# Kernel optimization log

Measured on AMD Instinct MI355X. Metric: run time of the kernel, lower is better.

The kernel has to match this reference:

```python
import jax, jax.numpy as jnp
import numpy as np

TEMPERATURE = 0.5
EPS = 1e-8  # matches torch cosine_similarity eps guard semantics (norm clamp)


def setup_inputs() -> dict:
    key = jax.random.key(0)
    k1, k2 = jax.random.split(key)
    B, D = 4096, 256
    z_i = jax.random.normal(k1, (B, D), dtype=jnp.float32)
    z_j = jax.random.normal(k2, (B, D), dtype=jnp.float32)
    return {"z_i": z_i, "z_j": z_j}


def reference(z_i, z_j):
    B = z_i.shape[0]
    z = jnp.concatenate([z_i, z_j], axis=0)            # [2B, D]
    # cosine similarity: normalize once, then GEMM
    norm = jnp.maximum(jnp.linalg.norm(z, axis=1, keepdims=True), EPS)
    zn = z / norm                                       # [2B, D]
    sim = zn @ zn.T                                     # [2B, 2B]
    # positives: diag(sim, +B) and diag(sim, -B)
    idx = jnp.arange(B)
    sim_ij = sim[idx, idx + B]
    sim_ji = sim[idx + B, idx]
    positives = jnp.concatenate([sim_ij, sim_ji])       # [2B]
    # masked denominator: exclude self-similarity
    mask = 1.0 - jnp.eye(2 * B, dtype=sim.dtype)
    denom = jnp.sum(mask * jnp.exp(sim / TEMPERATURE), axis=1)  # [2B]
    all_losses = -jnp.log(jnp.exp(positives / TEMPERATURE) / denom)
    return jnp.sum(all_losses) / (2 * B)
```

## Files before the change

### kernel.cpp

```cpp
#include <hip/hip_runtime.h>
#include <hip/hip_bf16.h>
#include <cstdint>
#include <cstddef>
#include <math.h>

#define D 256
#define TEMP_INV 2.0f
#define EPS_NORM 1e-8f
#define NTILES 2080

typedef __attribute__((ext_vector_type(8))) short bf16x8;
typedef __attribute__((ext_vector_type(4))) float f32x4;

__global__ void __launch_bounds__(256) normalize_rows(
    const float* __restrict__ zi, const float* __restrict__ zj,
    __hip_bfloat16* __restrict__ zn, float* __restrict__ out, int B) {
  const int wid = threadIdx.x >> 6;
  const int lane = threadIdx.x & 63;
  if (blockIdx.x == 0 && threadIdx.x == 0) out[0] = 0.0f;
#pragma unroll
  for (int it = 0; it < 4; ++it) {
    int row = it * 2048 + blockIdx.x * 4 + wid;
    const float* src = (row < B) ? (zi + (size_t)row * D)
                                 : (zj + (size_t)(row - B) * D);
    float4 v = ((const float4*)src)[lane];
    float ss = v.x * v.x + v.y * v.y + v.z * v.z + v.w * v.w;
    for (int off = 32; off; off >>= 1) ss += __shfl_xor(ss, off);
    float rn = 1.0f / fmaxf(sqrtf(ss), EPS_NORM);
    union { ushort4 u; __hip_bfloat16 h[4]; } o;
    o.h[0] = __float2bfloat16(v.x * rn);
    o.h[1] = __float2bfloat16(v.y * rn);
    o.h[2] = __float2bfloat16(v.z * rn);
    o.h[3] = __float2bfloat16(v.w * rn);
    ((ushort4*)zn)[(size_t)row * (D / 4) + lane] = o.u;
  }
}

__device__ __forceinline__ void decode_tile(int t, int Nb, int& by, int& bx) {
  float fb = (2.0f * Nb + 1.0f -
              sqrtf((float)((2 * Nb + 1) * (2 * Nb + 1) - 8 * t))) * 0.5f;
  int y = (int)fb;
  while ((y + 1) * Nb - ((y + 1) * y) / 2 <= t) ++y;
  while (y * Nb - (y * (y - 1)) / 2 > t) --y;
  by = y;
  bx = y + (t - (y * Nb - (y * (y - 1)) / 2));
}

__global__ void __launch_bounds__(256, 4) ntxent_gemm(
    const __hip_bfloat16* __restrict__ zn,
    float* __restrict__ part, float* __restrict__ pos, int B) {
  __shared__ __align__(16) __hip_bfloat16 Bsh[128 * 64];

  const int N = 2 * B;
  const int Nb = N / 128;
  int by, bx;
  decode_tile(blockIdx.x, Nb, by, bx);
  const int bm = by * 128;
  const int bn = bx * 128;
  const bool isDiag = (by == bx);
  const bool isPos = (bx == by + B / 128);

  const int tid = threadIdx.x;
  const int wid = tid >> 6;
  const int lane = tid & 63;
  const int wy = wid >> 1, wx = wid & 1;
  const int wrow0 = wid * 32;

  const int lr = lane >> 3;
  const int c8 = lane & 7;

  const int frow = lane & 15;
  const int quad = lane >> 4;
  const int f7 = frow & 7;

  f32x4 acc[4][4] = {};

  const __hip_bfloat16* gB = zn + (size_t)(bn + wrow0 + lr) * D + c8 * 8;
  const int ldsoff = (wrow0 + lr) * 64 + (c8 ^ lr) * 8;

  const __hip_bfloat16* gA = zn + (size_t)(bm + wy * 64 + frow) * D + quad * 8;

  float4 vb0 = *(const float4*)(gB + 0 * 8 * D);
  float4 vb1 = *(const float4*)(gB + 1 * 8 * D);
  float4 vb2 = *(const float4*)(gB + 2 * 8 * D);
  float4 vb3 = *(const float4*)(gB + 3 * 8 * D);

#pragma unroll
  for (int k0i = 0; k0i < 4; ++k0i) {
    __syncthreads();
    *(float4*)&Bsh[ldsoff + 0 * 8 * 64] = vb0;
    *(float4*)&Bsh[ldsoff + 1 * 8 * 64] = vb1;
    *(float4*)&Bsh[ldsoff + 2 * 8 * 64] = vb2;
    *(float4*)&Bsh[ldsoff + 3 * 8 * 64] = vb3;
    __syncthreads();
    if (k0i < 3) {
      const int k0 = (k0i + 1) * 64;
      vb0 = *(const float4*)(gB + 0 * 8 * D + k0);
      vb1 = *(const float4*)(gB + 1 * 8 * D + k0);
      vb2 = *(const float4*)(gB + 2 * 8 * D + k0);
      vb3 = *(const float4*)(gB + 3 * 8 * D + k0);
    }
#pragma unroll
    for (int kk = 0; kk < 2; ++kk) {
      const int kcol = k0i * 64 + kk * 32;
      bf16x8 a[4], b[4];
#pragma unroll
      for (int i = 0; i < 4; ++i)
        a[i] = *(const bf16x8*)(gA + (size_t)(i * 16) * D + kcol);
#pragma unroll
      for (int j = 0; j < 4; ++j)
        b[j] = *(const bf16x8*)
            &Bsh[(wx * 64 + j * 16 + frow) * 64 + ((kk * 4 + quad) ^ f7) * 8];
#pragma unroll
      for (int i = 0; i < 4; ++i)
#pragma unroll
        for (int j = 0; j < 4; ++j)
          acc[i][j] =
              __builtin_amdgcn_mfma_f32_16x16x32_bf16(a[i], b[j], acc[i][j], 0, 0, 0);
    }
  }

  __syncthreads();
  float* red = (float*)&Bsh[0];

  const int colq = lane & 15;
  float cs[4] = {0.0f, 0.0f, 0.0f, 0.0f};
#pragma unroll
  for (int i = 0; i < 4; ++i) {
#pragma unroll
    for (int r = 0; r < 4; ++r) {
      int rowloc = wy * 64 + i * 16 + quad * 4 + r;
      int row = bm + rowloc;
      float rs = 0.0f;
#pragma unroll
      for (int j = 0; j < 4; ++j) {
        int col = bn + wx * 64 + j * 16 + colq;
        float v = acc[i][j][r];
        float e = __expf(v * TEMP_INV);
        e = (isDiag && col == row) ? 0.0f : e;
        rs += e;
        cs[j] += e;
        if (isPos && col == row + B) { pos[row] = v; pos[col] = v; }
      }
      rs += __shfl_xor(rs, 1);
      rs += __shfl_xor(rs, 2);
      rs += __shfl_xor(rs, 4);
      rs += __shfl_xor(rs, 8);
      if (colq == 0) red[rowloc * 2 + wx] = rs;
    }
  }
#pragma unroll
  for (int j = 0; j < 4; ++j) {
    float c = cs[j];
    c += __shfl_xor(c, 16);
    c += __shfl_xor(c, 32);
    if (quad == 0) red[256 + (wx * 64 + j * 16 + colq) * 2 + wy] = c;
  }
  __syncthreads();
  if (tid < 128) {
    part[(size_t)bx * N + bm + tid] = red[tid * 2] + red[tid * 2 + 1];
  } else if (!isDiag) {
    int tt = tid - 128;
    part[(size_t)by * N + bn + tt] = red[256 + tt * 2] + red[256 + tt * 2 + 1];
  }
}

__global__ void __launch_bounds__(256) finalize(
    const float* __restrict__ part, const float* __restrict__ pos,
    float* __restrict__ out, int N) {
  const int idx = blockIdx.x * 256 + threadIdx.x;
  const int NS = N / 128;
  float s = 0.0f;
#pragma unroll 8
  for (int k = 0; k < NS; ++k) s += part[(size_t)k * N + idx];
  float loss = __logf(s) - pos[idx] * TEMP_INV;
  for (int off = 32; off; off >>= 1) loss += __shfl_xor(loss, off);
  __shared__ float redsh[4];
  if ((threadIdx.x & 63) == 0) redsh[threadIdx.x >> 6] = loss;
  __syncthreads();
  if (threadIdx.x == 0) {
    float tt = redsh[0] + redsh[1] + redsh[2] + redsh[3];
    atomicAdd(out, tt / (float)N);
  }
}

extern "C" void kernel_launch(void* const* d_in, const int* in_sizes, int n_in,
                              void* d_out, int out_size, void* d_ws, size_t ws_size,
                              hipStream_t stream) {
  const float* zi = (const float*)d_in[0];
  const float* zj = (const float*)d_in[1];
  const int B = in_sizes[0] / D;
  const int N = 2 * B;

  __hip_bfloat16* zn = (__hip_bfloat16*)d_ws;
  float* pos = (float*)((char*)d_ws + (size_t)N * D * sizeof(__hip_bfloat16));
  float* part = pos + N;

  normalize_rows<<<512, 256, 0, stream>>>(zi, zj, zn, (float*)d_out, B);
  ntxent_gemm<<<NTILES, 256, 0, stream>>>(zn, part, pos, B);
  finalize<<<N / 256, 256, 0, stream>>>(part, pos, (float*)d_out, N);
}
```

Baseline: 122.0 us.

## Drop LDS staging and write per-warp partial sums straight to global

The GEMM kernel stops staging the B tile through shared memory. Each warp now loads its B fragments directly from global memory, relying on the cache, and all __syncthreads barriers are gone. The row and column exp-sum reductions no longer pass through LDS. Each warp writes its partials to a partial-sum buffer twice as tall, and finalize sums N/64 slices instead of N/128. This removes barriers and LDS traffic, at the cost of redundant global/L2 reads of B across warps and twice the partial-sum writes and finalize reads, plus a larger workspace.

```diff
diff --git a/kernel.cpp b/kernel.cpp
--- a/kernel.cpp
+++ b/kernel.cpp
@@ -49,119 +49,83 @@
 __global__ void __launch_bounds__(256, 4) ntxent_gemm(
     const __hip_bfloat16* __restrict__ zn,
     float* __restrict__ part, float* __restrict__ pos, int B) {
-  __shared__ __align__(16) __hip_bfloat16 Bsh[128 * 64];
-
   const int N = 2 * B;
   const int Nb = N / 128;
   int by, bx;
   decode_tile(blockIdx.x, Nb, by, bx);
   const int bm = by * 128;
   const int bn = bx * 128;
-  const bool isDiag = (by == bx);
-  const bool isPos = (bx == by + B / 128);
 
   const int tid = threadIdx.x;
   const int wid = tid >> 6;
   const int lane = tid & 63;
   const int wy = wid >> 1, wx = wid & 1;
-  const int wrow0 = wid * 32;
-
-  const int lr = lane >> 3;
-  const int c8 = lane & 7;
 
   const int frow = lane & 15;
   const int quad = lane >> 4;
-  const int f7 = frow & 7;
+
+  const bool diagQ = (by == bx) && (wy == wx);
+  const bool posQ = (bx == by + B / 128) && (wy == wx);
+  const bool isDiag = (by == bx);
+
+  const __hip_bfloat16* gA = zn + (size_t)(bm + wy * 64 + frow) * D + quad * 8;
+  const __hip_bfloat16* gB = zn + (size_t)(bn + wx * 64 + frow) * D + quad * 8;
 
   f32x4 acc[4][4] = {};
 
-  const __hip_bfloat16* gB = zn + (size_t)(bn + wrow0 + lr) * D + c8 * 8;
-  const int ldsoff = (wrow0 + lr) * 64 + (c8 ^ lr) * 8;
-
-  const __hip_bfloat16* gA = zn + (size_t)(bm + wy * 64 + frow) * D + quad * 8;
-
-  float4 vb0 = *(const float4*)(gB + 0 * 8 * D);
-  float4 vb1 = *(const float4*)(gB + 1 * 8 * D);
-  float4 vb2 = *(const float4*)(gB + 2 * 8 * D);
-  float4 vb3 = *(const float4*)(gB + 3 * 8 * D);
-
 #pragma unroll
-  for (int k0i = 0; k0i < 4; ++k0i) {
-    __syncthreads();
-    *(float4*)&Bsh[ldsoff + 0 * 8 * 64] = vb0;
-    *(float4*)&Bsh[ldsoff + 1 * 8 * 64] = vb1;
-    *(float4*)&Bsh[ldsoff + 2 * 8 * 64] = vb2;
-    *(float4*)&Bsh[ldsoff + 3 * 8 * 64] = vb3;
-    __syncthreads();
-    if (k0i < 3) {
-      const int k0 = (k0i + 1) * 64;
-      vb0 = *(const float4*)(gB + 0 * 8 * D + k0);
-      vb1 = *(const float4*)(gB + 1 * 8 * D + k0);
-      vb2 = *(const float4*)(gB + 2 * 8 * D + k0);
-      vb3 = *(const float4*)(gB + 3 * 8 * D + k0);
-    }
+  for (int kc = 0; kc < 8; ++kc) {
+    const int kcol = kc * 32;
+    bf16x8 a[4], b[4];
 #pragma unroll
-    for (int kk = 0; kk < 2; ++kk) {
-      const int kcol = k0i * 64 + kk * 32;
-      bf16x8 a[4], b[4];
+    for (int i = 0; i < 4; ++i)
+      a[i] = *(const bf16x8*)(gA + (size_t)(i * 16) * D + kcol);
 #pragma unroll
-      for (int i = 0; i < 4; ++i)
-        a[i] = *(const bf16x8*)(gA + (size_t)(i * 16) * D + kcol);
+    for (int j = 0; j < 4; ++j)
+      b[j] = *(const bf16x8*)(gB + (size_t)(j * 16) * D + kcol);
+#pragma unroll
+    for (int i = 0; i < 4; ++i)
 #pragma unroll
       for (int j = 0; j < 4; ++j)
-        b[j] = *(const bf16x8*)
-            &Bsh[(wx * 64 + j * 16 + frow) * 64 + ((kk * 4 + quad) ^ f7) * 8];
-#pragma unroll
-      for (int i = 0; i < 4; ++i)
-#pragma unroll
-        for (int j = 0; j < 4; ++j)
-          acc[i][j] =
-              __builtin_amdgcn_mfma_f32_16x16x32_bf16(a[i], b[j], acc[i][j], 0, 0, 0);
-    }
+        acc[i][j] =
+            __builtin_amdgcn_mfma_f32_16x16x32_bf16(a[i], b[j], acc[i][j], 0, 0, 0);
   }
 
-  __syncthreads();
-  float* red = (float*)&Bsh[0];
-
-  const int colq = lane & 15;
+  const int colq = frow;
   float cs[4] = {0.0f, 0.0f, 0.0f, 0.0f};
 #pragma unroll
   for (int i = 0; i < 4; ++i) {
 #pragma unroll
     for (int r = 0; r < 4; ++r) {
-      int rowloc = wy * 64 + i * 16 + quad * 4 + r;
-      int row = bm + rowloc;
+      int rowoff = i * 16 + quad * 4 + r;
+      int row = bm + wy * 64 + rowoff;
       float rs = 0.0f;
 #pragma unroll
       for (int j = 0; j < 4; ++j) {
-        int col = bn + wx * 64 + j * 16 + colq;
+        int coloff = j * 16 + colq;
         float v = acc[i][j][r];
         float e = __expf(v * TEMP_INV);
-        e = (isDiag && col == row) ? 0.0f : e;
+        e = (diagQ && coloff == rowoff) ? 0.0f : e;
         rs += e;
         cs[j] += e;
-        if (isPos && col == row + B) { pos[row] = v; pos[col] = v; }
+        if (posQ && coloff == rowoff) { pos[row] = v; pos[row + B] = v; }
       }
       rs += __shfl_xor(rs, 1);
       rs += __shfl_xor(rs, 2);
       rs += __shfl_xor(rs, 4);
       rs += __shfl_xor(rs, 8);
-      if (colq == 0) red[rowloc * 2 + wx] = rs;
+      if (colq == 0) part[(size_t)(2 * bx + wx) * N + row] = rs;
     }
   }
+  if (!isDiag) {
 #pragma unroll
-  for (int j = 0; j < 4; ++j) {
-    float c = cs[j];
-    c += __shfl_xor(c, 16);
-    c += __shfl_xor(c, 32);
-    if (quad == 0) red[256 + (wx * 64 + j * 16 + colq) * 2 + wy] = c;
-  }
-  __syncthreads();
-  if (tid < 128) {
-    part[(size_t)bx * N + bm + tid] = red[tid * 2] + red[tid * 2 + 1];
-  } else if (!isDiag) {
-    int tt = tid - 128;
-    part[(size_t)by * N + bn + tt] = red[256 + tt * 2] + red[256 + tt * 2 + 1];
+    for (int j = 0; j < 4; ++j) {
+      float c = cs[j];
+      c += __shfl_xor(c, 16);
+      c += __shfl_xor(c, 32);
+      if (quad == 0)
+        part[(size_t)(2 * by + wy) * N + bn + wx * 64 + j * 16 + colq] = c;
+    }
   }
 }
 
@@ -169,9 +133,9 @@
     const float* __restrict__ part, const float* __restrict__ pos,
     float* __restrict__ out, int N) {
   const int idx = blockIdx.x * 256 + threadIdx.x;
-  const int NS = N / 128;
+  const int NS = N / 64;
   float s = 0.0f;
-#pragma unroll 8
+#pragma unroll 16
   for (int k = 0; k < NS; ++k) s += part[(size_t)k * N + idx];
   float loss = __logf(s) - pos[idx] * TEMP_INV;
   for (int off = 32; off; off >>= 1) loss += __shfl_xor(loss, off);
```

New measurement: 141.8 us. +16.3%, slower.
